# Performance work log

Hardware: AMD Instinct MI355X
Metric: run time of the kernel (lower is better)

The kernel has to match this reference:

```python
import jax, jax.numpy as jnp
import numpy as np

N = 10000   # nodes (Hi-C bins)
E = 640000  # directed edges
H = 2       # attention heads
C = 512     # per-head out channels
NEG_SLOPE = 0.2

def _leaky_relu(v):
    return jnp.where(v >= 0, v, NEG_SLOPE * v)

def setup_inputs() -> dict:
    key = jax.random.key(0)
    ks = jax.random.split(key, 16)
    s = 0.02
    return {
        "x": jax.random.normal(ks[0], (N, 512), jnp.float32),
        "edge_index": jax.random.randint(ks[1], (2, E), 0, N, dtype=jnp.int64),
        "W": jax.random.normal(ks[2], (512, H * C), jnp.float32) * s,
        "att_src": jax.random.normal(ks[3], (H, C), jnp.float32) * s,
        "att_dst": jax.random.normal(ks[4], (H, C), jnp.float32) * s,
        "bias_conv": jnp.zeros((H * C,), jnp.float32),
        "Wa": jax.random.normal(ks[5], (1024, 256), jnp.float32) * s,
        "ba": jnp.zeros((256,), jnp.float32),
        "W1": jax.random.normal(ks[6], (256, 128), jnp.float32) * s,
        "b1": jnp.zeros((128,), jnp.float32),
        "W2": jax.random.normal(ks[7], (128, 64), jnp.float32) * s,
        "b2": jnp.zeros((64,), jnp.float32),
        "W3": jax.random.normal(ks[8], (64, 3), jnp.float32) * s,
        "b3": jnp.zeros((3,), jnp.float32),
    }

def reference(x, edge_index, W, att_src, att_dst, bias_conv,
              Wa, ba, W1, b1, W2, b2, W3, b3):
    n = x.shape[0]
    # PyG GATConv default: add self loops
    loop = jnp.arange(n, dtype=edge_index.dtype)
    src = jnp.concatenate([edge_index[0], loop])  # [E+N]
    dst = jnp.concatenate([edge_index[1], loop])
    # linear projection -> [N, H, C]
    h = (x @ W).reshape(n, H, C)
    a_src = jnp.einsum('nhc,hc->nh', h, att_src)  # [N, H]
    a_dst = jnp.einsum('nhc,hc->nh', h, att_dst)
    e = _leaky_relu(a_src[src] + a_dst[dst])      # [E+N, H]
    # segment softmax over destination nodes
    m = jax.ops.segment_max(e, dst, num_segments=n)
    ex = jnp.exp(e - m[dst])
    denom = jax.ops.segment_sum(ex, dst, num_segments=n)
    alpha = ex / denom[dst]                        # [E+N, H]
    # weighted scatter-add aggregation
    out = jax.ops.segment_sum(h[src] * alpha[..., None], dst, num_segments=n)
    out = out.reshape(n, H * C) + bias_conv        # concat heads -> [N, 1024]
    # MLP (dropout is identity in eval)
    y = jax.nn.relu(out)
    y = jax.nn.relu(y @ Wa + ba)
    y = jax.nn.relu(y @ W1 + b1)
    y = jax.nn.relu(y @ W2 + b2)
    y = y @ W3 + b3                                # [N, 3]
    # cdist p=2 via gram trick, grad-safe sqrt at 0
    sq = jnp.sum(y * y, axis=1)
    d2 = jnp.maximum(sq[:, None] + sq[None, :] - 2.0 * (y @ y.T), 0.0)
    pos = d2 > 0
    return jnp.where(pos, jnp.sqrt(jnp.where(pos, d2, 1.0)), 0.0)  # [N, N]
```

## Files before the change

### kernel.cpp

```cpp
#include <hip/hip_runtime.h>
#include <hip/hip_bf16.h>
#include <math.h>

#define N_NODES 10000
#define NE      640000
#define NTOT    (NE + N_NODES)
#define HC      1024
#define CC      512
#define SLOT    256
#define CHN     (N_NODES * 64)

typedef __attribute__((ext_vector_type(8))) short bf16x8;
typedef __attribute__((ext_vector_type(4))) float f32x4;

__device__ __forceinline__ float lrelu(float v) { return v >= 0.f ? v : 0.2f * v; }

__device__ __forceinline__ void split1(float f, ushort& h, ushort& l) {
    unsigned u = __float_as_uint(f);
    unsigned hb = (u + 0x7FFFu + ((u >> 16) & 1u)) >> 16;
    float fh = __uint_as_float(hb << 16);
    float fl = f - fh;
    unsigned ul = __float_as_uint(fl);
    unsigned lb = (ul + 0x7FFFu + ((ul >> 16) & 1u)) >> 16;
    h = (ushort)hb; l = (ushort)lb;
}

__global__ __launch_bounds__(256) void transp_split(
    const float* __restrict__ Win, int K, int N,
    ushort* __restrict__ Th, ushort* __restrict__ Tl,
    float* __restrict__ zbuf, int zn)
{
    __shared__ float tile[32][33];
    int n0 = blockIdx.x * 32, k0 = blockIdx.y * 32;
    int tx = threadIdx.x & 31, ty = threadIdx.x >> 5;
    int gtid = (blockIdx.y * gridDim.x + blockIdx.x) * 256 + threadIdx.x;
    if (gtid < zn) zbuf[gtid] = 0.f;
    #pragma unroll
    for (int r = 0; r < 4; ++r)
        tile[ty + r * 8][tx] = Win[(size_t)(k0 + ty + r * 8) * N + n0 + tx];
    __syncthreads();
    #pragma unroll
    for (int r = 0; r < 4; ++r) {
        int n = ty + r * 8;
        float f = tile[tx][n];
        ushort h, l;
        split1(f, h, l);
        Th[(size_t)(n0 + n) * K + k0 + tx] = h;
        Tl[(size_t)(n0 + n) * K + k0 + tx] = l;
    }
}

template<int RELU_BIAS, int ATT, int SPLITA>
__global__ __launch_bounds__(256) void gemm_bf16x3(
    const ushort* __restrict__ Ah, const ushort* __restrict__ Al,
    const float* __restrict__ Af,
    const ushort* __restrict__ Bh, const ushort* __restrict__ Bl,
    const float* __restrict__ biasC,
    const float* __restrict__ attS, const float* __restrict__ attD,
    float* __restrict__ aS, float* __restrict__ aD,
    float* __restrict__ C, int M, int N, int K)
{
    __shared__ __align__(16) ushort sAh[4][128][8];
    __shared__ __align__(16) ushort sAl[4][128][8];
    __shared__ __align__(16) ushort sBh[4][128][8];
    __shared__ __align__(16) ushort sBl[4][128][8];
    const int bm = blockIdx.y * 128;
    const int bn = blockIdx.x * 128;
    const int tid = threadIdx.x;
    const int lane = tid & 63;
    const int w = tid >> 6;
    const int wm = (w >> 1) * 64, wn = (w & 1) * 64;
    const int l15 = lane & 15, l4 = lane >> 4;

    f32x4 acc[4][4];
    #pragma unroll
    for (int i = 0; i < 4; ++i)
        #pragma unroll
        for (int j = 0; j < 4; ++j)
            acc[i][j] = (f32x4){0.f, 0.f, 0.f, 0.f};

    for (int k0 = 0; k0 < K; k0 += 32) {
        #pragma unroll
        for (int qi = 0; qi < 4; ++qi) {
            int Q = qi * 256 + tid;
            int m = Q >> 3;
            int kq = (Q & 7) * 4;
            int gr = bm + m;
            ushort4 vh = make_ushort4(0, 0, 0, 0), vl = vh;
            if (SPLITA) {
                if (gr < M) {
                    float4 av = *(const float4*)(Af + (size_t)gr * K + k0 + kq);
                    split1(av.x, vh.x, vl.x);
                    split1(av.y, vh.y, vl.y);
                    split1(av.z, vh.z, vl.z);
                    split1(av.w, vh.w, vl.w);
                }
            } else if (gr < M) {
                vh = *(const ushort4*)(Ah + (size_t)gr * K + k0 + kq);
                vl = *(const ushort4*)(Al + (size_t)gr * K + k0 + kq);
            }
            *(ushort4*)&sAh[kq >> 3][m][kq & 7] = vh;
            *(ushort4*)&sAl[kq >> 3][m][kq & 7] = vl;
            ushort4 wh = *(const ushort4*)(Bh + (size_t)(bn + m) * K + k0 + kq);
            ushort4 wl = *(const ushort4*)(Bl + (size_t)(bn + m) * K + k0 + kq);
            *(ushort4*)&sBh[kq >> 3][m][kq & 7] = wh;
            *(ushort4*)&sBl[kq >> 3][m][kq & 7] = wl;
        }
        __syncthreads();
        bf16x8 ah[4], al[4], bh[4], bl[4];
        #pragma unroll
        for (int i = 0; i < 4; ++i) {
            ah[i] = *(const bf16x8*)&sAh[l4][wm + i * 16 + l15][0];
            al[i] = *(const bf16x8*)&sAl[l4][wm + i * 16 + l15][0];
            bh[i] = *(const bf16x8*)&sBh[l4][wn + i * 16 + l15][0];
            bl[i] = *(const bf16x8*)&sBl[l4][wn + i * 16 + l15][0];
        }
        #pragma unroll
        for (int i = 0; i < 4; ++i)
            #pragma unroll
            for (int j = 0; j < 4; ++j) {
                acc[i][j] = __builtin_amdgcn_mfma_f32_16x16x32_bf16(ah[i], bh[j], acc[i][j], 0, 0, 0);
                acc[i][j] = __builtin_amdgcn_mfma_f32_16x16x32_bf16(ah[i], bl[j], acc[i][j], 0, 0, 0);
                acc[i][j] = __builtin_amdgcn_mfma_f32_16x16x32_bf16(al[i], bh[j], acc[i][j], 0, 0, 0);
            }
        __syncthreads();
    }
    const int head = ATT ? ((bn + wn) >> 9) : 0;
    #pragma unroll
    for (int i = 0; i < 4; ++i) {
        #pragma unroll
        for (int r = 0; r < 4; ++r) {
            int row = bm + wm + i * 16 + l4 * 4 + r;
            if (row >= M) continue;
            float ps = 0.f, pd = 0.f;
            #pragma unroll
            for (int j = 0; j < 4; ++j) {
                int col = bn + wn + j * 16 + l15;
                float v = acc[i][j][r];
                if (RELU_BIAS) v = fmaxf(v + biasC[col], 0.f);
                if (ATT) {
                    C[(size_t)(col >> 6) * CHN + (size_t)row * 64 + (col & 63)] = v;
                    int cc = col & (CC - 1);
                    ps += v * attS[head * CC + cc];
                    pd += v * attD[head * CC + cc];
                } else {
                    C[(size_t)row * N + col] = v;
                }
            }
            if (ATT) {
                #pragma unroll
                for (int o = 1; o < 16; o <<= 1) {
                    ps += __shfl_xor(ps, o);
                    pd += __shfl_xor(pd, o);
                }
                if (l15 == 0) {
                    atomicAdd(&aS[row * 2 + head], ps);
                    atomicAdd(&aD[row * 2 + head], pd);
                }
            }
        }
    }
}

template<int RELU_OUT, int MLP3>
__global__ __launch_bounds__(256) void gemm64(
    const float* __restrict__ A, const float* __restrict__ B,
    const float* __restrict__ biasC, float* __restrict__ C,
    const float* __restrict__ W3, const float* __restrict__ b3,
    float4* __restrict__ y4,
    int M, int N, int K)
{
    __shared__ float As[16][68];
    __shared__ float Bs[16][68];
    const int bm = blockIdx.y * 64;
    const int bn = blockIdx.x * 64;
    const int tid = threadIdx.x;
    const int tx = tid & 15, ty = tid >> 4;

    const int arow  = tid >> 2;
    const int acol4 = (tid & 3) * 4;
    const int brow  = tid >> 4;
    const int bcol4 = (tid & 15) * 4;

    float acc[4][4] = {};

    for (int k0 = 0; k0 < K; k0 += 16) {
        int gr = bm + arow;
        float4 av = make_float4(0.f, 0.f, 0.f, 0.f);
        if (gr < M) av = *(const float4*)(A + (size_t)gr * K + k0 + acol4);
        As[acol4 + 0][arow] = av.x;
        As[acol4 + 1][arow] = av.y;
        As[acol4 + 2][arow] = av.z;
        As[acol4 + 3][arow] = av.w;
        float4 bv = *(const float4*)(B + (size_t)(k0 + brow) * N + bn + bcol4);
        *(float4*)&Bs[brow][bcol4] = bv;
        __syncthreads();
        #pragma unroll
        for (int k = 0; k < 16; ++k) {
            float a0 = As[k][ty * 4 + 0], a1 = As[k][ty * 4 + 1];
            float a2 = As[k][ty * 4 + 2], a3 = As[k][ty * 4 + 3];
            float b0 = Bs[k][tx * 4 + 0], b1 = Bs[k][tx * 4 + 1];
            float b2 = Bs[k][tx * 4 + 2], b3 = Bs[k][tx * 4 + 3];
            acc[0][0] += a0 * b0; acc[0][1] += a0 * b1; acc[0][2] += a0 * b2; acc[0][3] += a0 * b3;
            acc[1][0] += a1 * b0; acc[1][1] += a1 * b1; acc[1][2] += a1 * b2; acc[1][3] += a1 * b3;
            acc[2][0] += a2 * b0; acc[2][1] += a2 * b1; acc[2][2] += a2 * b2; acc[2][3] += a2 * b3;
            acc[3][0] += a3 * b0; acc[3][1] += a3 * b1; acc[3][2] += a3 * b2; acc[3][3] += a3 * b3;
        }
        __syncthreads();
    }
    #pragma unroll
    for (int i = 0; i < 4; ++i) {
        int row = bm + ty * 4 + i;
        if (row >= M) continue;
        if (MLP3) {
            float p0 = 0.f, p1 = 0.f, p2 = 0.f;
            #pragma unroll
            for (int j = 0; j < 4; ++j) {
                int col = tx * 4 + j;
                float v = fmaxf(acc[i][j] + biasC[col], 0.f);
                p0 += v * W3[col * 3 + 0];
                p1 += v * W3[col * 3 + 1];
                p2 += v * W3[col * 3 + 2];
            }
            #pragma unroll
            for (int o = 1; o < 16; o <<= 1) {
                p0 += __shfl_xor(p0, o);
                p1 += __shfl_xor(p1, o);
                p2 += __shfl_xor(p2, o);
            }
            if (tx == 0) {
                p0 += b3[0]; p1 += b3[1]; p2 += b3[2];
                y4[row] = make_float4(p0, p1, p2, p0 * p0 + p1 * p1 + p2 * p2);
            }
        } else {
            #pragma unroll
            for (int j = 0; j < 4; ++j) {
                int col = bn + tx * 4 + j;
                float v = acc[i][j] + biasC[col];
                if (RELU_OUT) v = fmaxf(v, 0.f);
                C[(size_t)row * N + col] = v;
            }
        }
    }
}

__global__ __launch_bounds__(256) void scatter_stats(
    const int* __restrict__ ei,
    const float2* __restrict__ a_src2, const float2* __restrict__ a_dst2,
    int* __restrict__ cnt,
    int2* __restrict__ pack0, int2* __restrict__ pack1)
{
    int e = blockIdx.x * blockDim.x + threadIdx.x;
    if (e >= NTOT) return;
    int s, d;
    if (e < NE) { s = ei[e]; d = ei[NE + e]; } else { s = d = e - NE; }
    float2 as = a_src2[s];
    float2 ad = a_dst2[d];
    float e0 = expf(lrelu(as.x + ad.x));
    float e1 = expf(lrelu(as.y + ad.y));
    int pos = atomicAdd(&cnt[d], 1);
    int slot = (d << 8) + pos;
    pack0[slot] = make_int2(s, __float_as_int(e0));
    pack1[slot] = make_int2(s, __float_as_int(e1));
}

__global__ __launch_bounds__(256) void aggregate_w4(
    const int* __restrict__ cnt,
    const int2* __restrict__ pack0, const int2* __restrict__ pack1,
    const float* __restrict__ bias_conv,
    const float* __restrict__ hc,
    ushort* __restrict__ outh, ushort* __restrict__ outl)
{
    int wave = threadIdx.x >> 6;
    int lane = threadIdx.x & 63;
    int g    = lane >> 4;
    int l16  = lane & 15;
    int d = blockIdx.x * 4 + wave;
    int chunk = blockIdx.y;
    int cb = chunk * 64;
    int hd = chunk >> 3;
    const int2* __restrict__ pk = ((hd == 0) ? pack0 : pack1) + (d << 8);
    int cd = cnt[d];
    const float* hbase = hc + (size_t)chunk * CHN + l16 * 4;
    float4 ac0 = make_float4(0.f, 0.f, 0.f, 0.f);
    float4 ac1 = make_float4(0.f, 0.f, 0.f, 0.f);
    float4 ac2 = make_float4(0.f, 0.f, 0.f, 0.f);
    float4 ac3 = make_float4(0.f, 0.f, 0.f, 0.f);
    float asum = 0.f;
    int i = g;
    for (; i + 12 < cd; i += 16) {
        int2 e0 = pk[i];
        int2 e1 = pk[i + 4];
        int2 e2 = pk[i + 8];
        int2 e3 = pk[i + 12];
        const float4 h0 = *(const float4*)(hbase + (size_t)e0.x * 64);
        const float4 h1 = *(const float4*)(hbase + (size_t)e1.x * 64);
        const float4 h2 = *(const float4*)(hbase + (size_t)e2.x * 64);
        const float4 h3 = *(const float4*)(hbase + (size_t)e3.x * 64);
        float a0 = __int_as_float(e0.y), a1 = __int_as_float(e1.y);
        float a2 = __int_as_float(e2.y), a3 = __int_as_float(e3.y);
        asum += a0 + a1 + a2 + a3;
        ac0.x += a0 * h0.x; ac0.y += a0 * h0.y; ac0.z += a0 * h0.z; ac0.w += a0 * h0.w;
        ac1.x += a1 * h1.x; ac1.y += a1 * h1.y; ac1.z += a1 * h1.z; ac1.w += a1 * h1.w;
        ac2.x += a2 * h2.x; ac2.y += a2 * h2.y; ac2.z += a2 * h2.z; ac2.w += a2 * h2.w;
        ac3.x += a3 * h3.x; ac3.y += a3 * h3.y; ac3.z += a3 * h3.z; ac3.w += a3 * h3.w;
    }
    for (; i < cd; i += 4) {
        int2 e0 = pk[i];
        float a0 = __int_as_float(e0.y);
        const float4 h0 = *(const float4*)(hbase + (size_t)e0.x * 64);
        asum += a0;
        ac0.x += a0 * h0.x; ac0.y += a0 * h0.y; ac0.z += a0 * h0.z; ac0.w += a0 * h0.w;
    }
    ac0.x += ac1.x + ac2.x + ac3.x;
    ac0.y += ac1.y + ac2.y + ac3.y;
    ac0.z += ac1.z + ac2.z + ac3.z;
    ac0.w += ac1.w + ac2.w + ac3.w;
    ac0.x += __shfl_xor(ac0.x, 16); ac0.y += __shfl_xor(ac0.y, 16);
    ac0.z += __shfl_xor(ac0.z, 16); ac0.w += __shfl_xor(ac0.w, 16);
    asum  += __shfl_xor(asum, 16);
    ac0.x += __shfl_xor(ac0.x, 32); ac0.y += __shfl_xor(ac0.y, 32);
    ac0.z += __shfl_xor(ac0.z, 32); ac0.w += __shfl_xor(ac0.w, 32);
    asum  += __shfl_xor(asum, 32);
    if (g == 0) {
        float inv = 1.f / asum;
        int c0 = cb + l16 * 4;
        float v[4];
        v[0] = fmaxf(ac0.x * inv + bias_conv[c0 + 0], 0.f);
        v[1] = fmaxf(ac0.y * inv + bias_conv[c0 + 1], 0.f);
        v[2] = fmaxf(ac0.z * inv + bias_conv[c0 + 2], 0.f);
        v[3] = fmaxf(ac0.w * inv + bias_conv[c0 + 3], 0.f);
        ushort hh[4], ll[4];
        #pragma unroll
        for (int j = 0; j < 4; ++j) split1(v[j], hh[j], ll[j]);
        *(ushort4*)(outh + (size_t)d * HC + c0) = make_ushort4(hh[0], hh[1], hh[2], hh[3]);
        *(ushort4*)(outl + (size_t)d * HC + c0) = make_ushort4(ll[0], ll[1], ll[2], ll[3]);
    }
}

__global__ __launch_bounds__(256) void pdist(
    const float4* __restrict__ y4, float* __restrict__ out)
{
    int i = blockIdx.y;
    int j0 = (blockIdx.x * 256 + threadIdx.x) * 4;
    if (j0 >= N_NODES) return;
    float4 yi = y4[i];
    float res[4];
    #pragma unroll
    for (int t = 0; t < 4; ++t) {
        float4 yj = y4[j0 + t];
        float d2 = yi.w + yj.w - 2.f * (yi.x * yj.x + yi.y * yj.y + yi.z * yj.z);
        d2 = fmaxf(d2, 0.f);
        res[t] = d2 > 0.f ? sqrtf(d2) : 0.f;
    }
    *(float4*)(out + (size_t)i * N_NODES + j0) = make_float4(res[0], res[1], res[2], res[3]);
}

extern "C" void kernel_launch(void* const* d_in, const int* in_sizes, int n_in,
                              void* d_out, int out_size, void* d_ws, size_t ws_size,
                              hipStream_t stream) {
    const float* x         = (const float*)d_in[0];
    const int*   ei        = (const int*)d_in[1];
    const float* W         = (const float*)d_in[2];
    const float* att_src   = (const float*)d_in[3];
    const float* att_dst   = (const float*)d_in[4];
    const float* bias_conv = (const float*)d_in[5];
    const float* Wa        = (const float*)d_in[6];
    const float* ba        = (const float*)d_in[7];
    const float* W1        = (const float*)d_in[8];
    const float* b1        = (const float*)d_in[9];
    const float* W2        = (const float*)d_in[10];
    const float* b2        = (const float*)d_in[11];
    const float* W3        = (const float*)d_in[12];
    const float* b3        = (const float*)d_in[13];
    float* out = (float*)d_out;

    float*  hc       = out;
    ushort* outh     = (ushort*)(out + 10240000);
    ushort* outl     = (ushort*)(out + 15360000);
    float*  y1       = out + 20480000;
    float*  y2       = out + 23040000;
    float*  a_src    = out + 24960000;
    float*  a_dst    = out + 24980000;
    int*    cnt      = (int*)(out + 25000000);
    int2*   pack0    = (int2*)(out + 25500000);
    int2*   pack1    = (int2*)(out + 30700000);
    ushort* Wth      = (ushort*)(out + 36000000);
    ushort* Wtl      = (ushort*)(out + 36300000);
    ushort* Wath     = (ushort*)(out + 36600000);
    ushort* Watl     = (ushort*)(out + 36800000);

    float4* y4 = (float4*)d_ws;

    transp_split<<<dim3(1024 / 32, 512 / 32), 256, 0, stream>>>(
        W, 512, 1024, Wth, Wtl, a_src, 50240);
    transp_split<<<dim3(256 / 32, 1024 / 32), 256, 0, stream>>>(
        Wa, 1024, 256, Wath, Watl, nullptr, 0);

    gemm_bf16x3<0, 1, 1><<<dim3(1024 / 128, (N_NODES + 127) / 128), 256, 0, stream>>>(
        nullptr, nullptr, x, Wth, Wtl, nullptr, att_src, att_dst, a_src, a_dst,
        hc, N_NODES, 1024, 512);

    scatter_stats<<<(NTOT + 255) / 256, 256, 0, stream>>>(
        ei, (const float2*)a_src, (const float2*)a_dst, cnt, pack0, pack1);

    aggregate_w4<<<dim3(N_NODES / 4, 16), 256, 0, stream>>>(
        cnt, pack0, pack1, bias_conv, hc, outh, outl);

    gemm_bf16x3<1, 0, 0><<<dim3(256 / 128, (N_NODES + 127) / 128), 256, 0, stream>>>(
        outh, outl, nullptr, Wath, Watl, ba, nullptr, nullptr, nullptr, nullptr,
        y1, N_NODES, 256, 1024);
    gemm64<1, 0><<<dim3(128 / 64, (N_NODES + 63) / 64), 256, 0, stream>>>(
        y1, W1, b1, y2, nullptr, nullptr, nullptr, N_NODES, 128, 256);
    gemm64<1, 1><<<dim3(1, (N_NODES + 63) / 64), 256, 0, stream>>>(
        y2, W2, b2, nullptr, W3, b3, y4, N_NODES, 64, 128);

    pdist<<<dim3((N_NODES + 1023) / 1024, N_NODES), 256, 0, stream>>>(y4, out);
}
```

Before: 513.8 us.

## Merge weight transpose kernels, prefetch edge packs, nontemporal pdist stores

Three separate changes. The two weight transpose/split launches become one 768-block launch that picks its matrix from the block index, saving one kernel launch. The aggregation loop now loads the next group of four packed edge entries before doing the FMAs on the current group, so index loads overlap the gathers, at the cost of more registers. The pdist kernel writes its 400 MB output with nontemporal stores to avoid polluting the cache.

```diff
diff --git a/kernel.cpp b/kernel.cpp
--- a/kernel.cpp
+++ b/kernel.cpp
@@ -25,16 +25,24 @@
     h = (ushort)hb; l = (ushort)lb;
 }
 
-__global__ __launch_bounds__(256) void transp_split(
-    const float* __restrict__ Win, int K, int N,
-    ushort* __restrict__ Th, ushort* __restrict__ Tl,
+__global__ __launch_bounds__(256) void transp_split2(
+    const float* __restrict__ W, ushort* __restrict__ Wth, ushort* __restrict__ Wtl,
+    const float* __restrict__ Wa, ushort* __restrict__ Wath, ushort* __restrict__ Watl,
     float* __restrict__ zbuf, int zn)
 {
     __shared__ float tile[32][33];
-    int n0 = blockIdx.x * 32, k0 = blockIdx.y * 32;
     int tx = threadIdx.x & 31, ty = threadIdx.x >> 5;
-    int gtid = (blockIdx.y * gridDim.x + blockIdx.x) * 256 + threadIdx.x;
-    if (gtid < zn) zbuf[gtid] = 0.f;
+    const float* Win; ushort* Th; ushort* Tl; int K, N, n0, k0;
+    if (blockIdx.x < 512) {
+        int gtid = blockIdx.x * 256 + threadIdx.x;
+        if (gtid < zn) zbuf[gtid] = 0.f;
+        Win = W;  Th = Wth;  Tl = Wtl;  K = 512;  N = 1024;
+        n0 = (blockIdx.x & 31) * 32;  k0 = (blockIdx.x >> 5) * 32;
+    } else {
+        int b = blockIdx.x - 512;
+        Win = Wa; Th = Wath; Tl = Watl; K = 1024; N = 256;
+        n0 = (b & 7) * 32;  k0 = (b >> 3) * 32;
+    }
     #pragma unroll
     for (int r = 0; r < 4; ++r)
         tile[ty + r * 8][tx] = Win[(size_t)(k0 + ty + r * 8) * N + n0 + tx];
@@ -288,22 +296,37 @@
     float4 ac3 = make_float4(0.f, 0.f, 0.f, 0.f);
     float asum = 0.f;
     int i = g;
-    for (; i + 12 < cd; i += 16) {
-        int2 e0 = pk[i];
-        int2 e1 = pk[i + 4];
-        int2 e2 = pk[i + 8];
-        int2 e3 = pk[i + 12];
-        const float4 h0 = *(const float4*)(hbase + (size_t)e0.x * 64);
-        const float4 h1 = *(const float4*)(hbase + (size_t)e1.x * 64);
-        const float4 h2 = *(const float4*)(hbase + (size_t)e2.x * 64);
-        const float4 h3 = *(const float4*)(hbase + (size_t)e3.x * 64);
-        float a0 = __int_as_float(e0.y), a1 = __int_as_float(e1.y);
-        float a2 = __int_as_float(e2.y), a3 = __int_as_float(e3.y);
-        asum += a0 + a1 + a2 + a3;
-        ac0.x += a0 * h0.x; ac0.y += a0 * h0.y; ac0.z += a0 * h0.z; ac0.w += a0 * h0.w;
-        ac1.x += a1 * h1.x; ac1.y += a1 * h1.y; ac1.z += a1 * h1.z; ac1.w += a1 * h1.w;
-        ac2.x += a2 * h2.x; ac2.y += a2 * h2.y; ac2.z += a2 * h2.z; ac2.w += a2 * h2.w;
-        ac3.x += a3 * h3.x; ac3.y += a3 * h3.y; ac3.z += a3 * h3.z; ac3.w += a3 * h3.w;
+    if (i + 12 < cd) {
+        int2 e0 = pk[i], e1 = pk[i + 4], e2 = pk[i + 8], e3 = pk[i + 12];
+        for (; i + 28 < cd; i += 16) {
+            const float4 h0 = *(const float4*)(hbase + (size_t)e0.x * 64);
+            const float4 h1 = *(const float4*)(hbase + (size_t)e1.x * 64);
+            const float4 h2 = *(const float4*)(hbase + (size_t)e2.x * 64);
+            const float4 h3 = *(const float4*)(hbase + (size_t)e3.x * 64);
+            int2 n0 = pk[i + 16], n1 = pk[i + 20], n2 = pk[i + 24], n3 = pk[i + 28];
+            float a0 = __int_as_float(e0.y), a1 = __int_as_float(e1.y);
+            float a2 = __int_as_float(e2.y), a3 = __int_as_float(e3.y);
+            asum += a0 + a1 + a2 + a3;
+            ac0.x += a0 * h0.x; ac0.y += a0 * h0.y; ac0.z += a0 * h0.z; ac0.w += a0 * h0.w;
+            ac1.x += a1 * h1.x; ac1.y += a1 * h1.y; ac1.z += a1 * h1.z; ac1.w += a1 * h1.w;
+            ac2.x += a2 * h2.x; ac2.y += a2 * h2.y; ac2.z += a2 * h2.z; ac2.w += a2 * h2.w;
+            ac3.x += a3 * h3.x; ac3.y += a3 * h3.y; ac3.z += a3 * h3.z; ac3.w += a3 * h3.w;
+            e0 = n0; e1 = n1; e2 = n2; e3 = n3;
+        }
+        {
+            const float4 h0 = *(const float4*)(hbase + (size_t)e0.x * 64);
+            const float4 h1 = *(const float4*)(hbase + (size_t)e1.x * 64);
+            const float4 h2 = *(const float4*)(hbase + (size_t)e2.x * 64);
+            const float4 h3 = *(const float4*)(hbase + (size_t)e3.x * 64);
+            float a0 = __int_as_float(e0.y), a1 = __int_as_float(e1.y);
+            float a2 = __int_as_float(e2.y), a3 = __int_as_float(e3.y);
+            asum += a0 + a1 + a2 + a3;
+            ac0.x += a0 * h0.x; ac0.y += a0 * h0.y; ac0.z += a0 * h0.z; ac0.w += a0 * h0.w;
+            ac1.x += a1 * h1.x; ac1.y += a1 * h1.y; ac1.z += a1 * h1.z; ac1.w += a1 * h1.w;
+            ac2.x += a2 * h2.x; ac2.y += a2 * h2.y; ac2.z += a2 * h2.z; ac2.w += a2 * h2.w;
+            ac3.x += a3 * h3.x; ac3.y += a3 * h3.y; ac3.z += a3 * h3.z; ac3.w += a3 * h3.w;
+            i += 16;
+        }
     }
     for (; i < cd; i += 4) {
         int2 e0 = pk[i];
@@ -353,7 +376,8 @@
         d2 = fmaxf(d2, 0.f);
         res[t] = d2 > 0.f ? sqrtf(d2) : 0.f;
     }
-    *(float4*)(out + (size_t)i * N_NODES + j0) = make_float4(res[0], res[1], res[2], res[3]);
+    f32x4 rv = {res[0], res[1], res[2], res[3]};
+    __builtin_nontemporal_store(rv, (f32x4*)(out + (size_t)i * N_NODES + j0));
 }
 
 extern "C" void kernel_launch(void* const* d_in, const int* in_sizes, int n_in,
@@ -392,10 +416,8 @@
 
     float4* y4 = (float4*)d_ws;
 
-    transp_split<<<dim3(1024 / 32, 512 / 32), 256, 0, stream>>>(
-        W, 512, 1024, Wth, Wtl, a_src, 50240);
-    transp_split<<<dim3(256 / 32, 1024 / 32), 256, 0, stream>>>(
-        Wa, 1024, 256, Wath, Watl, nullptr, 0);
+    transp_split2<<<768, 256, 0, stream>>>(
+        W, Wth, Wtl, Wa, Wath, Watl, a_src, 50240);
 
     gemm_bf16x3<0, 1, 1><<<dim3(1024 / 128, (N_NODES + 127) / 128), 256, 0, stream>>>(
         nullptr, nullptr, x, Wth, Wtl, nullptr, att_src, att_dst, a_src, a_dst,
```

Result: faster. 494.1 us (-3.8%).
